# Optimization experiments

Measured on AMD Instinct MI355X. Metric: run time of the kernel, lower is better.

The kernel has to match this reference:

```python
import jax, jax.numpy as jnp
import numpy as np

EPS_BN = 1e-5


def conv2d(x, w, b=None, pad=0, groups=1):
    y = jax.lax.conv_general_dilated(
        x, w, window_strides=(1, 1), padding=[(pad, pad), (pad, pad)],
        dimension_numbers=('NCHW', 'OIHW', 'NCHW'), feature_group_count=groups)
    if b is not None:
        y = y + b[None, :, None, None]
    return y


def bilinear_sample(x, py, px):
    # x: (C,H,W); py,px: (T,Ho,Wo) fractional sample coords. Zero outside borders
    # (matches torchvision deform_conv2d per-corner masking).
    C, H, W = x.shape
    xf = x.reshape(C, -1)
    y0 = jnp.floor(py)
    x0 = jnp.floor(px)

    def g(yi, xi):
        valid = (yi >= 0) & (yi <= H - 1) & (xi >= 0) & (xi <= W - 1)
        idx = (jnp.clip(yi, 0, H - 1).astype(jnp.int32) * W
               + jnp.clip(xi, 0, W - 1).astype(jnp.int32))
        v = xf[:, idx.reshape(-1)].reshape((C,) + idx.shape)  # (C,T,Ho,Wo)
        return jnp.where(valid[None], v, 0.0)

    wy1 = py - y0
    wx1 = px - x0
    wy0 = 1.0 - wy1
    wx0 = 1.0 - wx1
    return (g(y0, x0) * (wy0 * wx0)[None]
            + g(y0, x0 + 1.0) * (wy0 * wx1)[None]
            + g(y0 + 1.0, x0) * (wy1 * wx0)[None]
            + g(y0 + 1.0, x0 + 1.0) * (wy1 * wx1)[None])


def deform_depthwise(x, offset, dyn_w, k):
    # x: (B,C,H,W); offset: (B,2*k*k,H,W) interleaved (dy,dx) per tap;
    # dyn_w: (B,C,k,k) per-sample depthwise kernels. stride=1, pad=k//2.
    B, C, H, W = x.shape
    T = k * k
    pad = k // 2
    off = offset.reshape(B, T, 2, H, W)
    ky, kx = jnp.meshgrid(jnp.arange(k), jnp.arange(k), indexing='ij')
    base_y = (jnp.arange(H)[None, :, None] - pad
              + ky.reshape(T)[:, None, None]).astype(x.dtype)  # (T,H,1)
    base_x = (jnp.arange(W)[None, None, :] - pad
              + kx.reshape(T)[:, None, None]).astype(x.dtype)  # (T,1,W)
    py = base_y[None] + off[:, :, 0]  # (B,T,H,W)
    px = base_x[None] + off[:, :, 1]
    v = jax.vmap(bilinear_sample)(x, py, px)  # (B,C,T,H,W)
    return jnp.einsum('bct,bcthw->bchw', dyn_w.reshape(B, C, T), v)


def reference(F_c, dec_w, dec_b, off1_w, off1_b, off2_w, off2_b,
              akg_dw_w, akg_head_w, akg_head_b, pw2_w, pw2_b,
              bn_gamma, bn_beta):
    k = 3
    Kd = 7
    B, C, H, W = F_c.shape
    R = dec_w.shape[0]

    # TargetRegionDecoupler: F_i = F * M_i + F
    M = jax.nn.softmax(conv2d(F_c, dec_w, dec_b), axis=1)  # (B,R,H,W)

    outs = []
    for i in range(R):
        F_i = F_c * (1.0 + M[:, i:i + 1])
        # OffsetGenerator
        h = jax.nn.relu(conv2d(F_i, off1_w[i], off1_b[i], pad=1))
        p_i = conv2d(h, off2_w[i], off2_b[i], pad=1)  # (B,2*k*k,H,W)
        # AdaptiveKernelGenerator (exact adaptive pool: 56 -> 7 via 8x8 mean)
        d = F_i.reshape(B, C, Kd, H // Kd, Kd, W // Kd).mean(axis=(3, 5))
        d = jax.nn.relu(conv2d(d, akg_dw_w[i], None, pad=1, groups=C))
        d = d.mean(axis=(2, 3), keepdims=True)  # AdaptiveAvgPool2d(1)
        K_i = jnp.tanh(conv2d(d, akg_head_w[i], akg_head_b[i]).reshape(B, C, k, k))
        # per-sample dynamic depthwise deformable conv
        outs.append(deform_depthwise(F_i, p_i, K_i, k))

    O = conv2d(jnp.concatenate(outs, axis=1), pw2_w, pw2_b)
    # BatchNorm2d, training-mode batch statistics
    mean = O.mean(axis=(0, 2, 3), keepdims=True)
    var = O.var(axis=(0, 2, 3), keepdims=True)
    O = (O - mean) * jax.lax.rsqrt(var + EPS_BN)
    O = O * bn_gamma[None, :, None, None] + bn_beta[None, :, None, None]
    return O


def setup_inputs() -> dict:
    key = jax.random.key(0)
    ks = jax.random.split(key, 10)
    B, C, H, W = 8, 256, 56, 56
    k, R = 3, 2
    hid = max(32, C // 4)
    return {
        'F_c': jax.random.normal(ks[0], (B, C, H, W), jnp.float32),
        'dec_w': jax.random.normal(ks[1], (R, C, 1, 1), jnp.float32) * 0.1,
        'dec_b': jnp.zeros((R,), jnp.float32),
        'off1_w': jax.random.normal(ks[2], (R, hid, C, 3, 3), jnp.float32) * 0.05,
        'off1_b': jnp.zeros((R, hid), jnp.float32),
        'off2_w': jax.random.normal(ks[3], (R, 2 * k * k, hid, 3, 3), jnp.float32) * 0.01,
        'off2_b': jnp.zeros((R, 2 * k * k), jnp.float32),
        'akg_dw_w': jax.random.normal(ks[4], (R, C, 1, 3, 3), jnp.float32) * 0.1,
        'akg_head_w': jax.random.normal(ks[5], (R, C * k * k, C, 1, 1), jnp.float32) * 0.05,
        'akg_head_b': jnp.zeros((R, C * k * k), jnp.float32),
        'pw2_w': jax.random.normal(ks[6], (C, R * C, 1, 1), jnp.float32) * 0.05,
        'pw2_b': jnp.zeros((C,), jnp.float32),
        'bn_gamma': jnp.ones((C,), jnp.float32),
        'bn_beta': jnp.zeros((C,), jnp.float32),
    }
```

## Files before the change

### kernel.cpp

```cpp
#include <hip/hip_runtime.h>
#include <hip/hip_bf16.h>

#define BB 8
#define CC_ 256
#define HH 56
#define WW 56
#define HWSZ (HH*WW)
#define RR_ 2
#define HID 64
#define FPR ((size_t)8*58*58*256)
#define HPR ((size_t)8*58*58*64)
#define NPIX ((size_t)BB*HWSZ)

typedef __hip_bfloat16 bf16;
typedef __attribute__((ext_vector_type(8))) short short8;
typedef __attribute__((ext_vector_type(4))) short short4_t;
typedef __attribute__((ext_vector_type(4))) float f32x4;

struct Tap { int o00, o01, o10, o11; float w00, w01, w10, w11; };

__device__ __forceinline__ float b2f(bf16 v){ return __bfloat162float(v); }
__device__ __forceinline__ bf16 f2b(float v){ return __float2bfloat16(v); }
__device__ __forceinline__ float bs2f(short s){ return __uint_as_float(((unsigned)(unsigned short)s)<<16); }

__global__ __launch_bounds__(256) void k_scalepack(const float* __restrict__ F, const float* __restrict__ dec_w,
                                                   const float* __restrict__ dec_b,
                                                   bf16* __restrict__ Fp, float* __restrict__ rowsum){
    __shared__ float lds_f[256][57];
    __shared__ float lw0[256], lw1[256];
    __shared__ float ls0[56], ls1[56];
    int bx = blockIdx.x; int b = bx/HH, gy = bx%HH;
    int tid = threadIdx.x;
    lw0[tid] = dec_w[tid]; lw1[tid] = dec_w[CC_+tid];
    const float* Fb = F + (size_t)b*CC_*HWSZ + gy*WW;
    for (int it = 0; it < 56; ++it){
        int idx = it*256 + tid;
        int c = idx / 56, x = idx - c*56;
        lds_f[c][x] = Fb[(size_t)c*HWSZ + x];
    }
    __syncthreads();
    if (tid < 56){
        float a0 = dec_b[0], a1 = dec_b[1];
        for (int c = 0; c < CC_; ++c){ float v = lds_f[c][tid]; a0 += v*lw0[c]; a1 += v*lw1[c]; }
        float m = fmaxf(a0,a1);
        float e0 = __expf(a0-m), e1 = __expf(a1-m);
        float inv = 1.0f/(e0+e1);
        ls0[tid] = 1.0f + e0*inv; ls1[tid] = 1.0f + e1*inv;
    }
    __syncthreads();
    bf16 z = f2b(0.f);
    for (int r = 0; r < 2; ++r){
        const float* lsr = r ? ls1 : ls0;
        bf16* slab = Fp + (size_t)r*FPR + (size_t)b*58*58*256;
        bf16* dst = slab + ((size_t)(gy+1)*58 + 1)*256 + tid;
        for (int x2 = 0; x2 < 56; ++x2) dst[(size_t)x2*256] = f2b(lds_f[tid][x2] * lsr[x2]);
        float* rs = rowsum + ((((size_t)(r*8+b)*56 + gy)*7))*256 + tid;
        #pragma unroll
        for (int v = 0; v < 7; ++v){
            float sum = 0.f;
            #pragma unroll
            for (int k = 0; k < 8; ++k) sum += lds_f[tid][v*8+k] * lsr[v*8+k];
            rs[(size_t)v*256] = sum;
        }
        bf16* rowp = slab + (size_t)(gy+1)*58*256;
        rowp[tid] = z;
        rowp[57*256 + tid] = z;
        if (gy == 0){ for (int cidx = 0; cidx < 58; ++cidx) slab[(size_t)cidx*256 + tid] = z; }
        if (gy == 55){ bf16* r57 = slab + (size_t)57*58*256;
                       for (int cidx = 0; cidx < 58; ++cidx) r57[(size_t)cidx*256 + tid] = z; }
    }
}

__global__ void k_bprep_all(const float* __restrict__ w1, const float* __restrict__ wpw,
                            const float* __restrict__ wc2,
                            bf16* __restrict__ Bp, bf16* __restrict__ Bpw, bf16* __restrict__ Bc){
    int id = blockIdx.x;
    int L = threadIdx.x;
    if (id < 576){
        int nt = id & 3; id >>= 2; int icc = id & 7; id >>= 3; int t = id % 9; int r = id / 9;
        int oc = nt*16 + (L&15);
        const float* wr = w1 + (size_t)r*HID*CC_*9;
        bf16* out = Bp + (((((size_t)r*9 + t)*8 + icc)*4 + nt)*64 + L)*8;
        #pragma unroll
        for (int j = 0; j < 8; ++j){
            int ic = icc*32 + (L>>4)*8 + j;
            out[j] = f2b(wr[((size_t)oc*CC_ + ic)*9 + t]);
        }
    } else if (id < 832){
        id -= 576;
        int kk = id >> 4, nt = id & 15;
        int oc = nt*16 + (L&15);
        bf16* out = Bpw + (((size_t)(kk*16+nt))*64 + L)*8;
        #pragma unroll
        for (int j = 0; j < 8; ++j){
            int ic = kk*32 + (L>>4)*8 + j;
            out[j] = f2b(wpw[(size_t)oc*512 + ic]);
        }
    } else {
        id -= 832;
        int nt = id & 1; id >>= 1; int ks = id % 18; int r = id / 18;
        int t = ks >> 1, chunk = ks & 1;
        int oc = nt*16 + (L&15);
        const float* wr = wc2 + (size_t)r*18*HID*9;
        bf16* out = Bc + ((((size_t)r*18 + ks)*2 + nt)*64 + L)*8;
        #pragma unroll
        for (int j = 0; j < 8; ++j){
            int ic = chunk*32 + (L>>4)*8 + j;
            out[j] = (oc < 18) ? f2b(wr[((size_t)oc*HID + ic)*9 + t]) : f2b(0.f);
        }
    }
}

__global__ __launch_bounds__(256, 4) void k_conv1(const bf16* __restrict__ Fp, const bf16* __restrict__ Bp,
                                                  const float* __restrict__ bias, bf16* __restrict__ hp){
    __shared__ __attribute__((aligned(16))) bf16 blds[16384];
    int bx = blockIdx.x; int b = bx & 7; int rid = bx >> 3; int yp = rid % 28; int r = rid / 28;
    int y0 = yp*2;
    int tid = threadIdx.x; int wave = tid>>6, lane = tid&63;
    int m = lane&15, q = lane>>4;
    int x0 = (wave==3) ? 40 : wave*16;
    f32x4 acc[2][4];
    #pragma unroll
    for (int i=0;i<2;++i)
        #pragma unroll
        for (int j=0;j<4;++j) acc[i][j] = (f32x4){0,0,0,0};
    const bf16* Fb = Fp + (size_t)r*FPR + ((size_t)b*58*58)*256;
    const bf16* Bpr = Bp + (size_t)r*9*16384;
    short8 pf[8];
    #pragma unroll
    for (int j = 0; j < 8; ++j) pf[j] = *(const short8*)(Bpr + (size_t)(j*256 + tid)*8);
    #pragma unroll 1
    for (int t = 0; t < 9; ++t){
        __syncthreads();
        #pragma unroll
        for (int j = 0; j < 8; ++j) *(short8*)&blds[(j*256 + tid)*8] = pf[j];
        __syncthreads();
        if (t < 8){
            const bf16* src = Bpr + (size_t)(t+1)*16384;
            #pragma unroll
            for (int j = 0; j < 8; ++j) pf[j] = *(const short8*)(src + (size_t)(j*256 + tid)*8);
        }
        int ty = t/3, tx = t%3;
        const bf16* arow = Fb + ((size_t)(y0+ty)*58 + (x0+m+tx))*256 + q*8;
        #pragma unroll
        for (int icc = 0; icc < 8; ++icc){
            short8 a0 = *(const short8*)(arow + icc*32);
            short8 a1 = *(const short8*)(arow + 58*256 + icc*32);
            const bf16* bb = &blds[icc*2048 + lane*8];
            short8 b0 = *(const short8*)(bb);
            short8 b1 = *(const short8*)(bb + 512);
            short8 b2 = *(const short8*)(bb + 1024);
            short8 b3 = *(const short8*)(bb + 1536);
            acc[0][0] = __builtin_amdgcn_mfma_f32_16x16x32_bf16(a0, b0, acc[0][0], 0, 0, 0);
            acc[1][0] = __builtin_amdgcn_mfma_f32_16x16x32_bf16(a1, b0, acc[1][0], 0, 0, 0);
            acc[0][1] = __builtin_amdgcn_mfma_f32_16x16x32_bf16(a0, b1, acc[0][1], 0, 0, 0);
            acc[1][1] = __builtin_amdgcn_mfma_f32_16x16x32_bf16(a1, b1, acc[1][1], 0, 0, 0);
            acc[0][2] = __builtin_amdgcn_mfma_f32_16x16x32_bf16(a0, b2, acc[0][2], 0, 0, 0);
            acc[1][2] = __builtin_amdgcn_mfma_f32_16x16x32_bf16(a1, b2, acc[1][2], 0, 0, 0);
            acc[0][3] = __builtin_amdgcn_mfma_f32_16x16x32_bf16(a0, b3, acc[0][3], 0, 0, 0);
            acc[1][3] = __builtin_amdgcn_mfma_f32_16x16x32_bf16(a1, b3, acc[1][3], 0, 0, 0);
        }
    }
    const float* br = bias + r*HID;
    bf16* slab = hp + (size_t)r*HPR + (size_t)b*58*58*64;
    bf16 z = f2b(0.f);
    #pragma unroll
    for (int rr = 0; rr < 2; ++rr){
        int y = y0 + rr;
        bf16* hrow = slab + ((size_t)(y+1)*58 + 1)*64;
        #pragma unroll
        for (int nt = 0; nt < 4; ++nt){
            int oc = nt*16 + m;
            float bv = br[oc];
            #pragma unroll
            for (int r2 = 0; r2 < 4; ++r2){
                int x = x0 + q*4 + r2;
                hrow[(size_t)x*64 + oc] = f2b(fmaxf(acc[rr][nt][r2] + bv, 0.f));
            }
        }
        bf16* rowp = slab + (size_t)(y+1)*58*64;
        if (tid < 64) rowp[tid] = z;
        else if (tid < 128) rowp[57*64 + (tid-64)] = z;
        if (y == 0){ for (int idx = tid; idx < 58*64; idx += 256) slab[idx] = z; }
        if (y == 55){ bf16* r57 = slab + (size_t)57*58*64;
                      for (int idx = tid; idx < 58*64; idx += 256) r57[idx] = z; }
    }
}

__global__ __launch_bounds__(256) void k_conv2m(const bf16* __restrict__ hp, const bf16* __restrict__ Bc,
                                                const float* __restrict__ bias, Tap* __restrict__ tap){
    __shared__ float pld[18][56];
    int bx = blockIdx.x; int b = bx & 7; int rid = bx >> 3; int y = rid % 56; int r = rid / 56;
    int tid = threadIdx.x; int wave = tid>>6, lane = tid&63;
    int m = lane&15, q = lane>>4;
    int x0 = (wave==3) ? 40 : wave*16;
    f32x4 acc0 = {0,0,0,0}, acc1 = {0,0,0,0};
    const bf16* Hb = hp + (size_t)r*HPR + ((size_t)b*58 + y)*58*64;
    const bf16* Bcr = Bc + (size_t)r*18*2*64*8;
    #pragma unroll
    for (int t = 0; t < 9; ++t){
        int ty = t/3, tx = t%3;
        const bf16* arow = Hb + ((size_t)ty*58 + (x0+m+tx))*64 + q*8;
        #pragma unroll
        for (int chunk = 0; chunk < 2; ++chunk){
            short8 a = *(const short8*)(arow + chunk*32);
            const bf16* bb = Bcr + (((size_t)(t*2+chunk))*2*64 + lane)*8;
            short8 b0 = *(const short8*)(bb);
            short8 b1 = *(const short8*)(bb + 64*8);
            acc0 = __builtin_amdgcn_mfma_f32_16x16x32_bf16(a, b0, acc0, 0, 0, 0);
            acc1 = __builtin_amdgcn_mfma_f32_16x16x32_bf16(a, b1, acc1, 0, 0, 0);
        }
    }
    const float* br = bias + r*18;
    #pragma unroll
    for (int r2 = 0; r2 < 4; ++r2){
        int x = x0 + q*4 + r2;
        pld[m][x] = acc0[r2] + br[m];
        if (m < 2) pld[16+m][x] = acc1[r2] + br[16+m];
    }
    __syncthreads();
    for (int e = tid; e < 504; e += 256){
        int t = e / 56, x = e % 56;
        int ky = t / 3, kx = t % 3;
        float dy = pld[2*t][x];
        float dx = pld[2*t+1][x];
        float py = (float)(y - 1 + ky) + dy;
        float px = (float)(x - 1 + kx) + dx;
        float y0f = floorf(py), x0f = floorf(px);
        float wy1 = py - y0f, wx1 = px - x0f;
        float wy0 = 1.f - wy1, wx0 = 1.f - wx1;
        float vy0 = (y0f >= 0.f  && y0f <= 55.f) ? 1.f : 0.f;
        float vy1 = (y0f >= -1.f && y0f <= 54.f) ? 1.f : 0.f;
        float vx0 = (x0f >= 0.f  && x0f <= 55.f) ? 1.f : 0.f;
        float vx1 = (x0f >= -1.f && x0f <= 54.f) ? 1.f : 0.f;
        int yy0 = (int)y0f, x0i = (int)x0f;
        int iy0 = min(max(yy0,0),55),   iy1 = min(max(yy0+1,0),55);
        int ix0 = min(max(x0i,0),55),   ix1 = min(max(x0i+1,0),55);
        Tap td;
        td.o00 = ((iy0+1)*58 + ix0+1)*256;
        td.o01 = ((iy0+1)*58 + ix1+1)*256;
        td.o10 = ((iy1+1)*58 + ix0+1)*256;
        td.o11 = ((iy1+1)*58 + ix1+1)*256;
        td.w00 = wy0*wx0*vy0*vx0;
        td.w01 = wy0*wx1*vy0*vx1;
        td.w10 = wy1*wx0*vy1*vx0;
        td.w11 = wy1*wx1*vy1*vx1;
        size_t pid = ((size_t)(r*8 + b))*3136 + y*56 + x;
        tap[pid*9 + t] = td;
    }
}

__global__ __launch_bounds__(256) void k_akg_s(const float* __restrict__ rowsum, const float* __restrict__ dw,
                                               float* __restrict__ s){
    int rb = blockIdx.x; int r = rb >> 3;
    int c = threadIdx.x;
    const float* rs = rowsum + ((size_t)rb*56*7)*256 + c;
    float d[7][7];
    #pragma unroll
    for (int u = 0; u < 7; ++u)
        #pragma unroll
        for (int v = 0; v < 7; ++v){
            float acc = 0.f;
            #pragma unroll
            for (int k = 0; k < 8; ++k) acc += rs[(size_t)((u*8+k)*7 + v)*256];
            d[u][v] = acc * (1.f/64.f);
        }
    const float* wp = dw + (size_t)r*CC_*9 + c*9;
    float w[9];
    #pragma unroll
    for (int k = 0; k < 9; ++k) w[k] = wp[k];
    float tot = 0.f;
    #pragma unroll
    for (int u = 0; u < 7; ++u)
        #pragma unroll
        for (int v = 0; v < 7; ++v){
            float acc = 0.f;
            #pragma unroll
            for (int ky = 0; ky < 3; ++ky){
                int uu = u+ky-1; if ((unsigned)uu >= 7u) continue;
                #pragma unroll
                for (int kx = 0; kx < 3; ++kx){
                    int vv = v+kx-1; if ((unsigned)vv >= 7u) continue;
                    acc += d[uu][vv]*w[ky*3+kx];
                }
            }
            tot += fmaxf(acc, 0.f);
        }
    s[(size_t)rb*CC_ + c] = tot * (1.f/49.f);
}

__global__ void k_akg_head(const float* __restrict__ s, const float* __restrict__ hw,
                           const float* __restrict__ hb, float* __restrict__ Kw){
    int gid = blockIdx.x; int r = gid / 72; int id = gid % 72;
    int b = id / 9; int og = id % 9;
    __shared__ float sv[CC_];
    int tid = threadIdx.x;
    sv[tid] = s[(size_t)(r*8+b)*CC_ + tid];
    __syncthreads();
    int o = og*256 + tid;
    const float* wp = hw + (size_t)r*2304*CC_ + (size_t)o*CC_;
    float acc = hb[(size_t)r*2304 + o];
    for (int c2=0;c2<CC_;++c2) acc += wp[c2]*sv[c2];
    int c = o / 9, t = o - 9*c;
    Kw[((size_t)r*BB + b)*2304 + t*256 + c] = tanhf(acc);
}

__global__ __launch_bounds__(256, 8) void k_deform(const bf16* __restrict__ Fp, const Tap* __restrict__ tap,
                                                   const float* __restrict__ Kw, bf16* __restrict__ outsN){
    __shared__ float klds[2432];
    __shared__ Tap tlds[4][18];
    int bx = blockIdx.x; int b = bx & 7; int rest = bx >> 3;
    int pg = rest % 392; int creg = rest / 392;
    int tid = threadIdx.x; int w = tid >> 6, l = tid & 63;
    int wu = __builtin_amdgcn_readfirstlane(w);
    int yx0 = pg*8 + wu*2;
    size_t slab = (size_t)(creg*8 + b)*3136;
    const float* Kb = Kw + ((size_t)creg*8 + b)*2304;
    for (int i = tid*4; i < 2304; i += 1024){
        f32x4 v = *(const f32x4*)(Kb + i);
        int t = i >> 8, rem = i & 255;
        *(f32x4*)&klds[(rem >> 3)*76 + t*8 + (rem & 4)] = v;
    }
    if (l < 36)
        *(f32x4*)((char*)&tlds[wu][0] + l*16) =
            *(const f32x4*)((const char*)(tap + (slab + yx0)*9) + l*16);
    __syncthreads();
    int h = l >> 5, li = l & 31;
    const bf16* Fb = Fp + (size_t)creg*FPR + (size_t)b*58*58*256;
    int c0 = li*8;
    const float* kl = &klds[li*76];
    const Tap* tw = &tlds[wu][h*9];
    float acc[8];
    #pragma unroll
    for (int j = 0; j < 8; ++j) acc[j] = 0.f;
    #pragma unroll 3
    for (int t = 0; t < 9; ++t){
        Tap d = tw[t];
        short8 f00 = *(const short8*)(Fb + d.o00 + c0);
        short8 f01 = *(const short8*)(Fb + d.o01 + c0);
        short8 f10 = *(const short8*)(Fb + d.o10 + c0);
        short8 f11 = *(const short8*)(Fb + d.o11 + c0);
        f32x4 klo = *(const f32x4*)(kl + t*8);
        f32x4 khi = *(const f32x4*)(kl + t*8 + 4);
        #pragma unroll
        for (int j = 0; j < 4; ++j){
            float v = d.w00*bs2f(f00[j]) + d.w01*bs2f(f01[j]) + d.w10*bs2f(f10[j]) + d.w11*bs2f(f11[j]);
            acc[j] += klo[j]*v;
        }
        #pragma unroll
        for (int j = 4; j < 8; ++j){
            float v = d.w00*bs2f(f00[j]) + d.w01*bs2f(f01[j]) + d.w10*bs2f(f10[j]) + d.w11*bs2f(f11[j]);
            acc[j] += khi[j-4]*v;
        }
    }
    __attribute__((aligned(16))) bf16 tmp[8];
    #pragma unroll
    for (int j = 0; j < 8; ++j) tmp[j] = f2b(acc[j]);
    *(short8*)(outsN + ((size_t)b*HWSZ + yx0 + h)*512 + creg*256 + c0) = *(const short8*)tmp;
}

__global__ __launch_bounds__(256) void k_pw2_mstats(const bf16* __restrict__ outsN, const bf16* __restrict__ Bpw,
                                                    const float* __restrict__ bias, float* __restrict__ stats,
                                                    float* __restrict__ O){
    __shared__ float ls[2][2][256];
    int tid = threadIdx.x; int wave = tid>>6, lane = tid&63;
    int pixGroup = wave>>1, ntH = wave&1;
    int m = lane&15, q = lane>>4;
    size_t pb = (size_t)blockIdx.x*64 + pixGroup*32;
    const bf16* Ap0 = outsN + (pb + m)*512 + q*8;
    const bf16* Ap1 = Ap0 + (size_t)16*512;
    f32x4 acc[2][8];
    #pragma unroll
    for (int g=0;g<2;++g)
        #pragma unroll
        for (int i=0;i<8;++i) acc[g][i] = (f32x4){0,0,0,0};
    #pragma unroll 1
    for (int kk = 0; kk < 16; ++kk){
        short8 a0 = *(const short8*)(Ap0 + kk*32);
        short8 a1 = *(const short8*)(Ap1 + kk*32);
        const bf16* Bk = Bpw + (((size_t)kk*16 + ntH*8)*64 + lane)*8;
        #pragma unroll
        for (int nt2 = 0; nt2 < 8; ++nt2){
            short8 b = *(const short8*)(Bk + (size_t)nt2*64*8);
            acc[0][nt2] = __builtin_amdgcn_mfma_f32_16x16x32_bf16(a0, b, acc[0][nt2], 0, 0, 0);
            acc[1][nt2] = __builtin_amdgcn_mfma_f32_16x16x32_bf16(a1, b, acc[1][nt2], 0, 0, 0);
        }
    }
    #pragma unroll
    for (int nt2 = 0; nt2 < 8; ++nt2){
        int oc = ntH*128 + nt2*16 + m;
        float bv = bias[oc];
        float s1 = 0.f, s2 = 0.f;
        #pragma unroll
        for (int g = 0; g < 2; ++g){
            size_t pbg = pb + g*16;
            int b_idx = (int)(pbg / HWSZ);
            int yx0 = (int)(pbg % HWSZ);
            float* op = O + ((size_t)b_idx*CC_ + oc)*HWSZ + yx0 + q*4;
            #pragma unroll
            for (int r = 0; r < 4; ++r){
                float v = acc[g][nt2][r] + bv;
                op[r] = v;
                s1 += v; s2 += v*v;
            }
        }
        s1 += __shfl_down(s1, 32); s1 += __shfl_down(s1, 16);
        s2 += __shfl_down(s2, 32); s2 += __shfl_down(s2, 16);
        if (q == 0){ ls[pixGroup][0][oc] = s1; ls[pixGroup][1][oc] = s2; }
    }
    __syncthreads();
    if (tid < 256){
        atomicAdd(&stats[tid],       ls[0][0][tid] + ls[1][0][tid]);
        atomicAdd(&stats[256 + tid], ls[0][1][tid] + ls[1][1][tid]);
    }
}

__global__ __launch_bounds__(256) void k_bnapply(const float* __restrict__ O, const float* __restrict__ stats,
                                                 const float* __restrict__ gamma, const float* __restrict__ beta,
                                                 float* __restrict__ out){
    int n = (blockIdx.x*256 + threadIdx.x)*4;
    int c = (n / HWSZ) % CC_;
    float ninv = 1.f/(float)NPIX;
    float mean = stats[c]*ninv;
    float var = fmaxf(stats[256+c]*ninv - mean*mean, 0.f);
    float rsq = rsqrtf(var + 1e-5f);
    float g = gamma[c], be = beta[c];
    f32x4 v = *(const f32x4*)(O + n);
    f32x4 o;
    #pragma unroll
    for (int j = 0; j < 4; ++j) o[j] = (v[j] - mean)*rsq*g + be;
    *(f32x4*)(out + n) = o;
}

extern "C" void kernel_launch(void* const* d_in, const int* in_sizes, int n_in,
                              void* d_out, int out_size, void* d_ws, size_t ws_size,
                              hipStream_t stream) {
    (void)in_sizes; (void)n_in; (void)out_size; (void)ws_size;
    const float* F_c    = (const float*)d_in[0];
    const float* dec_w  = (const float*)d_in[1];
    const float* dec_b  = (const float*)d_in[2];
    const float* off1_w = (const float*)d_in[3];
    const float* off1_b = (const float*)d_in[4];
    const float* off2_w = (const float*)d_in[5];
    const float* off2_b = (const float*)d_in[6];
    const float* akg_dw = (const float*)d_in[7];
    const float* akg_hw = (const float*)d_in[8];
    const float* akg_hb = (const float*)d_in[9];
    const float* pw2_w  = (const float*)d_in[10];
    const float* pw2_b  = (const float*)d_in[11];
    const float* gamma  = (const float*)d_in[12];
    const float* beta   = (const float*)d_in[13];
    float* out = (float*)d_out;

    char* ws = (char*)d_ws;
    size_t off = 0;
    auto alloc = [&](size_t bytes)->char*{
        char* r = ws + off;
        off = (off + bytes + 255) & ~(size_t)255;
        return r;
    };
    bf16*  Fp    = (bf16*) alloc(2*FPR*2);
    bf16*  Bp    = (bf16*) alloc((size_t)2*9*8*4*64*8*2);
    bf16*  Bpw   = (bf16*) alloc((size_t)16*16*64*8*2);
    bf16*  Bc    = (bf16*) alloc((size_t)2*18*2*64*8*2);
    float* rowsum= (float*)alloc((size_t)2*8*56*7*256*4);
    bf16*  hp    = (bf16*) alloc(2*HPR*2);
    float* s     = (float*)alloc((size_t)2*BB*CC_*4);
    float* Kw    = (float*)alloc((size_t)2*BB*CC_*9*4);
    bf16*  outsN = (bf16*) alloc(NPIX*512*2);
    Tap*   tap   = (Tap*)  alloc((size_t)2*NPIX*9*sizeof(Tap));
    float* stats = (float*)alloc(2*CC_*4);
    float* O = (float*)Fp;

    hipMemsetAsync(stats, 0, 2*CC_*sizeof(float), stream);

    k_scalepack<<<dim3(BB*HH), dim3(256), 0, stream>>>(F_c, dec_w, dec_b, Fp, rowsum);
    k_bprep_all<<<dim3(904), dim3(64), 0, stream>>>(off1_w, pw2_w, off2_w, Bp, Bpw, Bc);

    k_conv1<<<dim3(2*BB*28), dim3(256), 0, stream>>>(Fp, Bp, off1_b, hp);
    k_conv2m<<<dim3(2*BB*HH), dim3(256), 0, stream>>>(hp, Bc, off2_b, tap);
    k_akg_s<<<dim3(16), dim3(256), 0, stream>>>(rowsum, akg_dw, s);
    k_akg_head<<<dim3(2*BB*9), dim3(256), 0, stream>>>(s, akg_hw, akg_hb, Kw);
    k_deform<<<dim3(2*BB*392), dim3(256), 0, stream>>>(Fp, tap, Kw, outsN);

    k_pw2_mstats<<<dim3(392), dim3(256), 0, stream>>>(outsN, Bpw, pw2_b, stats, O);
    k_bnapply<<<dim3((int)(NPIX*CC_/1024)), dim3(256), 0, stream>>>(O, stats, gamma, beta, out);
}
```

Measured before the change: 265.8 us.

## Stage conv1 input rows in LDS and remap blocks for weight locality

The conv1 kernel now copies the four padded input rows (58 pixels x 256 channels, padded to 264 to avoid bank conflicts) into shared memory once, instead of reading A fragments from global memory for each of the 9 taps. The block index mapping also changes so that neighbouring blocks share the same region weights and row. The cost is about 120KB of LDS per block, and launch bounds drop to one block per SM, so occupancy falls and less latency can be hidden.

```diff
diff --git a/kernel.cpp b/kernel.cpp
--- a/kernel.cpp
+++ b/kernel.cpp
@@ -111,10 +111,15 @@
     }
 }
 
-__global__ __launch_bounds__(256, 4) void k_conv1(const bf16* __restrict__ Fp, const bf16* __restrict__ Bp,
+__global__ __launch_bounds__(256, 1) void k_conv1(const bf16* __restrict__ Fp, const bf16* __restrict__ Bp,
                                                   const float* __restrict__ bias, bf16* __restrict__ hp){
+    __shared__ __attribute__((aligned(16))) bf16 alds[4*58*264];
     __shared__ __attribute__((aligned(16))) bf16 blds[16384];
-    int bx = blockIdx.x; int b = bx & 7; int rid = bx >> 3; int yp = rid % 28; int r = rid / 28;
+    int bx = blockIdx.x;
+    int x8 = bx & 7, g = bx >> 3;
+    int r = x8 >> 2;
+    int b = (g/28)*4 + (x8 & 3);
+    int yp = g % 28;
     int y0 = yp*2;
     int tid = threadIdx.x; int wave = tid>>6, lane = tid&63;
     int m = lane&15, q = lane>>4;
@@ -129,6 +134,25 @@
     short8 pf[8];
     #pragma unroll
     for (int j = 0; j < 8; ++j) pf[j] = *(const short8*)(Bpr + (size_t)(j*256 + tid)*8);
+    const bf16* FbA = Fb + (size_t)y0*58*256;
+    for (int kb = 0; kb < 4; ++kb){
+        short8 v[8];
+        #pragma unroll
+        for (int j = 0; j < 8; ++j){
+            int k = kb*8 + j;
+            if (k < 29) v[j] = *(const short8*)(FbA + (size_t)k*2048 + tid*8);
+        }
+        #pragma unroll
+        for (int j = 0; j < 8; ++j){
+            int k = kb*8 + j;
+            if (k < 29){
+                int e = k*2048 + tid*8;
+                int xl = e >> 8, c = e & 255;
+                int row = xl / 58, x = xl - row*58;
+                *(short8*)&alds[row*15312 + x*264 + c] = v[j];
+            }
+        }
+    }
     #pragma unroll 1
     for (int t = 0; t < 9; ++t){
         __syncthreads();
@@ -141,11 +165,11 @@
             for (int j = 0; j < 8; ++j) pf[j] = *(const short8*)(src + (size_t)(j*256 + tid)*8);
         }
         int ty = t/3, tx = t%3;
-        const bf16* arow = Fb + ((size_t)(y0+ty)*58 + (x0+m+tx))*256 + q*8;
+        int abase = ty*15312 + (x0+m+tx)*264 + q*8;
         #pragma unroll
         for (int icc = 0; icc < 8; ++icc){
-            short8 a0 = *(const short8*)(arow + icc*32);
-            short8 a1 = *(const short8*)(arow + 58*256 + icc*32);
+            short8 a0 = *(const short8*)&alds[abase + icc*32];
+            short8 a1 = *(const short8*)&alds[abase + 15312 + icc*32];
             const bf16* bb = &blds[icc*2048 + lane*8];
             short8 b0 = *(const short8*)(bb);
             short8 b1 = *(const short8*)(bb + 512);
```

Measured after the change: 258.6 us. 2.7% less time.
